# Performance work log

Measured on AMD Instinct MI355X. Metric: run time of the kernel, lower is better.

Reference implementation:

```python
import jax, jax.numpy as jnp
import numpy as np

B, C, H, W = 2, 512, 64, 64
S = 2            # scale_factor
HEADS = 8
GROUPS = 32      # assumed GroupNorm groups for group_norm(in_channels)
DK = C // HEADS
SCALE = 1.0 / DK ** 2   # faithful to source: 1/d_k**2
RES = H // S
R = RES * 2 - 1


def setup_inputs() -> dict:
    key = jax.random.key(0)
    ks = jax.random.split(key, 8)
    f = lambda k, shp, s=0.02: jax.random.normal(k, shp, jnp.float32) * s
    return {
        "x": jax.random.normal(ks[0], (B, C, H, W), jnp.float32),
        "q_w": f(ks[1], (C, C, 1, 1)),
        "q_b": jnp.zeros((C,), jnp.float32),
        "kv_w": f(ks[2], (2 * C, C, 1, 1)),
        "kv_b": jnp.zeros((2 * C,), jnp.float32),
        "off1_w": f(ks[3], (C, C, S, S)),
        "off1_b": jnp.zeros((C,), jnp.float32),
        "gn_w": jnp.ones((C,), jnp.float32),
        "gn_b": jnp.zeros((C,), jnp.float32),
        "off2_w": f(ks[4], (2, C, 1, 1)),
        "rpe_table": f(ks[5], (HEADS, R, R), 0.01),
        "proj_w": f(ks[6], (C, C, 1, 1)),
        "proj_b": jnp.zeros((C,), jnp.float32),
    }


def _conv(x, w, b=None, stride=1):
    y = jax.lax.conv_general_dilated(x, w, (stride, stride), 'VALID',
                                     dimension_numbers=('NCHW', 'OIHW', 'NCHW'))
    return y if b is None else y + b[None, :, None, None]


def _group_norm(x, w, b, eps=1e-5):
    n, c, h, wd = x.shape
    xg = x.reshape(n, GROUPS, -1)
    mu = xg.mean(-1, keepdims=True)
    var = xg.var(-1, keepdims=True)
    xg = (xg - mu) * jax.lax.rsqrt(var + eps)
    return xg.reshape(n, c, h, wd) * w[None, :, None, None] + b[None, :, None, None]


def _grid_sample(img, grid):
    # bilinear, align_corners=True; img [B,C,H,W], grid [B,...,2] in (x,y) order
    Bn, Cn, Hn, Wn = img.shape
    gshape = grid.shape[1:-1]
    g = grid.reshape(Bn, -1, 2)
    x = (g[..., 0] + 1.0) * 0.5 * (Wn - 1)
    y = (g[..., 1] + 1.0) * 0.5 * (Hn - 1)
    x0 = jnp.floor(x); y0 = jnp.floor(y)
    wx = (x - x0)[:, None, :]; wy = (y - y0)[:, None, :]
    x0i = jnp.clip(x0.astype(jnp.int32), 0, Wn - 1)
    x1i = jnp.clip(x0i + 1, 0, Wn - 1)
    y0i = jnp.clip(y0.astype(jnp.int32), 0, Hn - 1)
    y1i = jnp.clip(y0i + 1, 0, Hn - 1)
    imf = img.reshape(Bn, Cn, Hn * Wn)
    gat = lambda yi, xi: jnp.take_along_axis(imf, (yi * Wn + xi)[:, None, :], axis=2)
    out = (gat(y0i, x0i) * (1 - wx) * (1 - wy) + gat(y0i, x1i) * wx * (1 - wy)
           + gat(y1i, x0i) * (1 - wx) * wy + gat(y1i, x1i) * wx * wy)
    return out.reshape(Bn, Cn, *gshape)


def _forward(x, q_w, q_b, kv_w, kv_b, off1_w, off1_b, gn_w, gn_b, off2_w,
             rpe_table, proj_w, proj_b):
    l = H * W
    q = _conv(x, q_w, q_b)                                   # [B,C,H,W]
    t = _conv(q, off1_w, off1_b, stride=S)                   # [B,C,h,w]
    t = jax.nn.gelu(_group_norm(t, gn_w, gn_b), approximate=False)
    offset = _conv(t, off2_w).transpose(0, 2, 3, 1)          # [B,h,w,2] (y,x)
    h, w = offset.shape[1], offset.shape[2]
    n = h * w
    # reference points (linspace 0.5..h-0.5, normalized by h-1)
    ry = (jnp.linspace(0.5, h - 0.5, h) / (h - 1.0)) * 2.0 - 1.0
    rx = (jnp.linspace(0.5, w - 0.5, w) / (w - 1.0)) * 2.0 - 1.0
    ref = jnp.stack(jnp.meshgrid(ry, rx, indexing='ij'), -1)  # [h,w,2]
    pos = jnp.clip(offset + ref[None], -1.0, 1.0)             # [B,h,w,2]
    sampled = _grid_sample(x, pos[..., ::-1])                 # [B,C,h,w] (context=x)
    kv = _conv(sampled.reshape(B, C, 1, n), kv_w, kv_b)       # [B,2C,1,n]
    k, v = kv[:, :C], kv[:, C:]
    qf = q.reshape(B * HEADS, DK, l)
    kf = k.reshape(B * HEADS, DK, n)
    vf = v.reshape(B * HEADS, DK, n)
    attn = jnp.einsum('bcm,bcn->bmn', qf, kf) * SCALE         # [B*H, l, n]
    # query grid (arange, normalized by dim-1)
    gy = jnp.arange(H, dtype=jnp.float32) / (H - 1.0) * 2.0 - 1.0
    gx = jnp.arange(W, dtype=jnp.float32) / (W - 1.0) * 2.0 - 1.0
    qg = jnp.stack(jnp.meshgrid(gy, gx, indexing='ij'), -1).reshape(l, 2)
    disp = (qg[None, :, None, :] - pos.reshape(B, 1, n, 2)) * 0.5  # [B,l,n,2]
    rpe = jnp.broadcast_to(rpe_table[None], (B, HEADS, R, R))
    bias = _grid_sample(rpe, disp[..., ::-1])                  # [B,HEADS,l,n]
    attn = jax.nn.softmax(attn + bias.reshape(B * HEADS, l, n), axis=-1)
    out = jnp.einsum('bmn,bcn->bcm', attn, vf).reshape(B, C, H, W)
    return _conv(out, proj_w, proj_b)


def reference(x, q_w, q_b, kv_w, kv_b, off1_w, off1_b, gn_w, gn_b, off2_w,
              rpe_table, proj_w, proj_b):
    return _forward(x, q_w, q_b, kv_w, kv_b, off1_w, off1_b, gn_w, gn_b,
                    off2_w, rpe_table, proj_w, proj_b)
```

## Files before the change

kernel.cpp:

```cpp
#include <hip/hip_runtime.h>
#include <hip/hip_bf16.h>
#include <hip/hip_fp16.h>
#include <math.h>

typedef float floatx4 __attribute__((ext_vector_type(4)));
typedef short shortx8 __attribute__((ext_vector_type(8)));
typedef unsigned short ush;

#define NB    2
#define NC    512
#define NL    4096
#define NN    1024
#define NH    8
#define NDK   64
#define NR    63
#define LOG2E 1.44269504f
#define QT_SCALE (1.44269504f/4096.0f)

#define OFF_QT     0u
#define OFF_T      2097152u
#define OFF_GS     3145728u
#define OFF_POS    3145856u
#define OFF_KT     3149952u
#define OFF_VV     3674240u
#define OFF_SMP    4198528u
#define OFF_WEFF   4722816u
#define OFF_BEFF   5771392u
#define OFF_PART   5771904u
#define OFF_AO     5771904u

__device__ __forceinline__ ush f2bf(float f) {
    unsigned u = __float_as_uint(f);
    u += 0x7fffu + ((u >> 16) & 1u);
    return (ush)(u >> 16);
}
__device__ __forceinline__ float bf2f(ush h) {
    return __uint_as_float(((unsigned)h) << 16);
}

template<int NP, int BSRC, int OUTMODE>
__global__ __launch_bounds__(256) void gemm_mfma_k(
    const float* __restrict__ A, const void* __restrict__ Bv,
    const float* __restrict__ bias, void* __restrict__ Yv, void* __restrict__ Y2,
    int M, int K, int P, int KS)
{
    __shared__ ush a_hi[128 * 72];
    __shared__ ush b_hi[64 * 72];
    __shared__ ush a_lo[NP == 3 ? 128 * 72 : 64];
    __shared__ ush b_lo[NP == 3 ? 64 * 72 : 64];

    int tid = threadIdx.x;
    int wv = tid >> 6, lane = tid & 63, quad = lane >> 4, l15 = lane & 15;
    int bz = blockIdx.z;
    int b = bz / KS, ks = bz - b * KS;
    int m0 = blockIdx.y * 128, p0 = blockIdx.x * 64;
    int Ksl = K / KS, kbeg = ks * Ksl;

    floatx4 acc[2][4];
    #pragma unroll
    for (int mt = 0; mt < 2; ++mt)
        #pragma unroll
        for (int pt = 0; pt < 4; ++pt) acc[mt][pt] = (floatx4)0.f;

    for (int kc = 0; kc < Ksl; kc += 64) {
        int kg0 = kbeg + kc;
        #pragma unroll
        for (int r = 0; r < 8; ++r) {
            int idx = r * 256 + tid;
            int m = idx >> 4, k4 = (idx & 15) << 2;
            float4 av = *(const float4*)(A + (size_t)(m0 + m) * K + kg0 + k4);
            int o = m * 72 + k4;
            ush h0 = f2bf(av.x), h1 = f2bf(av.y), h2 = f2bf(av.z), h3 = f2bf(av.w);
            a_hi[o] = h0; a_hi[o + 1] = h1; a_hi[o + 2] = h2; a_hi[o + 3] = h3;
            if (NP == 3) {
                a_lo[o]     = f2bf(av.x - bf2f(h0));
                a_lo[o + 1] = f2bf(av.y - bf2f(h1));
                a_lo[o + 2] = f2bf(av.z - bf2f(h2));
                a_lo[o + 3] = f2bf(av.w - bf2f(h3));
            }
        }
        #pragma unroll
        for (int r = 0; r < 8; ++r) {
            int idx = r * 256 + tid;
            int k = idx >> 5, p2 = (idx & 31) << 1;
            float v0, v1;
            if (BSRC == 0) {
                const float* Bp = (const float*)Bv + (size_t)b * K * P;
                float2 t2 = *(const float2*)(Bp + (size_t)(kg0 + k) * P + p0 + p2);
                v0 = t2.x; v1 = t2.y;
            } else if (BSRC == 1) {
                const float* Bp = (const float*)Bv + (size_t)b * NC * NL;
                int kk = kg0 + k;
                int c = kk >> 2, kh = (kk >> 1) & 1, kw = kk & 1;
                int p = p0 + p2;
                int oh = p >> 5, ow = p & 31;
                const float* base = Bp + (size_t)c * NL + (2 * oh + kh) * 64 + kw;
                v0 = base[2 * ow];
                v1 = base[2 * ow + 2];
            } else {
                const ush* Bp = (const ush*)Bv + (size_t)b * K * P;
                unsigned u = *(const unsigned*)(Bp + (size_t)(kg0 + k) * P + p0 + p2);
                v0 = bf2f((ush)(u & 0xffffu));
                v1 = bf2f((ush)(u >> 16));
            }
            ush h0 = f2bf(v0), h1 = f2bf(v1);
            b_hi[p2 * 72 + k] = h0;
            b_hi[(p2 + 1) * 72 + k] = h1;
            if (NP == 3) {
                b_lo[p2 * 72 + k]       = f2bf(v0 - bf2f(h0));
                b_lo[(p2 + 1) * 72 + k] = f2bf(v1 - bf2f(h1));
            }
        }
        __syncthreads();

        shortx8 ah[2][2], al[2][2];
        #pragma unroll
        for (int mt = 0; mt < 2; ++mt)
            #pragma unroll
            for (int kk = 0; kk < 2; ++kk) {
                int o = (wv * 32 + mt * 16 + l15) * 72 + kk * 32 + quad * 8;
                ah[mt][kk] = *(const shortx8*)&a_hi[o];
                if (NP == 3) al[mt][kk] = *(const shortx8*)&a_lo[o];
            }
        #pragma unroll
        for (int pt = 0; pt < 4; ++pt) {
            #pragma unroll
            for (int kk = 0; kk < 2; ++kk) {
                int o = (pt * 16 + l15) * 72 + kk * 32 + quad * 8;
                shortx8 bh = *(const shortx8*)&b_hi[o];
                acc[0][pt] = __builtin_amdgcn_mfma_f32_16x16x32_bf16(ah[0][kk], bh, acc[0][pt], 0, 0, 0);
                acc[1][pt] = __builtin_amdgcn_mfma_f32_16x16x32_bf16(ah[1][kk], bh, acc[1][pt], 0, 0, 0);
                if (NP == 3) {
                    shortx8 bl = *(const shortx8*)&b_lo[o];
                    acc[0][pt] = __builtin_amdgcn_mfma_f32_16x16x32_bf16(ah[0][kk], bl, acc[0][pt], 0, 0, 0);
                    acc[1][pt] = __builtin_amdgcn_mfma_f32_16x16x32_bf16(ah[1][kk], bl, acc[1][pt], 0, 0, 0);
                    acc[0][pt] = __builtin_amdgcn_mfma_f32_16x16x32_bf16(al[0][kk], bh, acc[0][pt], 0, 0, 0);
                    acc[1][pt] = __builtin_amdgcn_mfma_f32_16x16x32_bf16(al[1][kk], bh, acc[1][pt], 0, 0, 0);
                }
            }
        }
        __syncthreads();
    }

    #pragma unroll
    for (int mt = 0; mt < 2; ++mt) {
        #pragma unroll
        for (int reg = 0; reg < 4; ++reg) {
            int m = m0 + wv * 32 + mt * 16 + quad * 4 + reg;
            float bb = (OUTMODE == 2) ? 0.f : bias[m];
            #pragma unroll
            for (int pt = 0; pt < 4; ++pt) {
                int p = p0 + pt * 16 + l15;
                float val = acc[mt][pt][reg] + bb;
                if (OUTMODE == 0) {
                    ((float*)Yv)[(size_t)b * M * P + (size_t)m * P + p] = val;
                } else if (OUTMODE == 2) {
                    ((float*)Yv)[(size_t)(ks * NB + b) * M * P + (size_t)m * P + p] = val;
                } else if (OUTMODE == 5) {
                    int h = m >> 6, d = m & 63;
                    ((ush*)Yv)[(((size_t)(b * 8 + h) * 4096) + p) * 64 + d] = f2bf(val * QT_SCALE);
                } else {
                    if (m < 512) {
                        int h = m >> 6, d = m & 63;
                        ((ush*)Yv)[(((size_t)(b * 8 + h) * 1024) + p) * 64 + d] = f2bf(val);
                    } else {
                        int c = m - 512;
                        ((ush*)Y2)[((size_t)(b * 512) + c) * 1024 + p] = f2bf(val);
                    }
                }
            }
        }
    }
}

__global__ __launch_bounds__(256) void weff_k(
    const float* __restrict__ off1w, const float* __restrict__ qw,
    float* __restrict__ weff)
{
    int ci = blockIdx.x * 256 + threadIdx.x;
    int co0 = blockIdx.y * 4;
    float acc[4][4] = {};
    #pragma unroll 4
    for (int cm = 0; cm < 512; ++cm) {
        float qv = qw[(size_t)cm * 512 + ci];
        #pragma unroll
        for (int c = 0; c < 4; ++c) {
            float4 w4 = *(const float4*)(off1w + ((size_t)(co0 + c) * 512 + cm) * 4);
            acc[c][0] += w4.x * qv;
            acc[c][1] += w4.y * qv;
            acc[c][2] += w4.z * qv;
            acc[c][3] += w4.w * qv;
        }
    }
    #pragma unroll
    for (int c = 0; c < 4; ++c)
        #pragma unroll
        for (int khw = 0; khw < 4; ++khw)
            weff[(size_t)(co0 + c) * 2048 + ci * 4 + khw] = acc[c][khw];
}

__global__ __launch_bounds__(256) void biaseff_k(const float* __restrict__ off1w,
                                                 const float* __restrict__ off1b,
                                                 const float* __restrict__ qb,
                                                 float* __restrict__ beff)
{
    int co = blockIdx.x;
    int tid = threadIdx.x;
    float s = 0.f;
    #pragma unroll
    for (int r = 0; r < 2; ++r) {
        int cm = r * 256 + tid;
        float4 w = *(const float4*)(off1w + ((size_t)co * 512 + cm) * 4);
        s += (w.x + w.y + w.z + w.w) * qb[cm];
    }
    #pragma unroll
    for (int off = 32; off >= 1; off >>= 1) s += __shfl_xor(s, off);
    __shared__ float red[4];
    if ((tid & 63) == 0) red[tid >> 6] = s;
    __syncthreads();
    if (tid == 0) beff[co] = off1b[co] + red[0] + red[1] + red[2] + red[3];
}

__global__ __launch_bounds__(256) void reduce_off1_k(const float* __restrict__ part,
                                                     const float* __restrict__ beff,
                                                     float* __restrict__ t)
{
    int i = blockIdx.x * 256 + threadIdx.x;
    float v = part[i] + part[i + 1048576] + part[i + 2097152] + part[i + 3145728];
    t[i] = v + beff[(i >> 10) & 511];
}

__global__ __launch_bounds__(256) void gn_stats_k(const float* __restrict__ T, float* __restrict__ gs)
{
    int bg = blockIdx.x;
    const float* base = T + (size_t)bg * 16384;
    float s = 0.f, ss = 0.f;
    for (int i = threadIdx.x; i < 16384; i += 256) { float v = base[i]; s += v; ss += v * v; }
    #pragma unroll
    for (int off = 32; off >= 1; off >>= 1) { s += __shfl_xor(s, off); ss += __shfl_xor(ss, off); }
    __shared__ float red[8];
    int wv = threadIdx.x >> 6;
    if ((threadIdx.x & 63) == 0) { red[wv * 2] = s; red[wv * 2 + 1] = ss; }
    __syncthreads();
    if (threadIdx.x == 0) {
        float S = red[0] + red[2] + red[4] + red[6];
        float SS = red[1] + red[3] + red[5] + red[7];
        float mu = S / 16384.f;
        float var = SS / 16384.f - mu * mu;
        gs[bg * 2] = mu;
        gs[bg * 2 + 1] = rsqrtf(var + 1e-5f);
    }
}

__global__ __launch_bounds__(256) void gn_gelu_k(float* __restrict__ T, const float* __restrict__ gs,
                                                 const float* __restrict__ gw, const float* __restrict__ gb)
{
    int idx = blockIdx.x * 256 + threadIdx.x;
    int bg = idx >> 14;
    int c = (idx >> 10) & 511;
    float mu = gs[bg * 2], rs = gs[bg * 2 + 1];
    float v = (T[idx] - mu) * rs * gw[c] + gb[c];
    T[idx] = v * 0.5f * (1.f + erff(v * 0.70710678118654752f));
}

__global__ __launch_bounds__(256) void offset_pos_k(const float* __restrict__ T,
                                                    const float* __restrict__ w2,
                                                    float* __restrict__ pos)
{
    int b = blockIdx.x >> 5;
    int og = threadIdx.x & 31;
    int cg = threadIdx.x >> 5;
    int op = ((blockIdx.x & 31) << 5) + og;
    const float* Tb = T + (size_t)b * NC * NN + (size_t)cg * 64 * NN + op;
    float o0 = 0.f, o1 = 0.f;
    #pragma unroll 4
    for (int c = 0; c < 64; ++c) {
        float tv = Tb[(size_t)c * NN];
        o0 += w2[cg * 64 + c] * tv;
        o1 += w2[512 + cg * 64 + c] * tv;
    }
    __shared__ float rs[2][8][32];
    rs[0][cg][og] = o0;
    rs[1][cg][og] = o1;
    __syncthreads();
    if (threadIdx.x < 64) {
        int coord = threadIdx.x >> 5, og2 = threadIdx.x & 31;
        float s = 0.f;
        #pragma unroll
        for (int k = 0; k < 8; ++k) s += rs[coord][k][og2];
        int opf = ((blockIdx.x & 31) << 5) + og2;
        int oh = opf >> 5, ow = opf & 31;
        float ref = (coord == 0) ? ((0.5f + oh) / 31.f * 2.f - 1.f)
                                 : ((0.5f + ow) / 31.f * 2.f - 1.f);
        pos[((size_t)b * 1024 + opf) * 2 + coord] = fminf(fmaxf(s + ref, -1.f), 1.f);
    }
}

__global__ __launch_bounds__(256) void sample_k(const float* __restrict__ x,
                                                const float* __restrict__ pos,
                                                ush* __restrict__ smp)
{
    int idx = blockIdx.x * 256 + threadIdx.x;
    int j = idx & 1023, c = (idx >> 10) & 511, b = idx >> 19;
    float py = pos[(b * 1024 + j) * 2];
    float px = pos[(b * 1024 + j) * 2 + 1];
    float fx = (px + 1.f) * 0.5f * 63.f;
    float fy = (py + 1.f) * 0.5f * 63.f;
    float flx = floorf(fx), fly = floorf(fy);
    float wx = fx - flx, wy = fy - fly;
    int x0 = min(max((int)flx, 0), 63), y0 = min(max((int)fly, 0), 63);
    int x1 = min(x0 + 1, 63),           y1 = min(y0 + 1, 63);
    const float* xb = x + ((size_t)(b * NC + c)) * NL;
    float v00 = xb[y0 * 64 + x0];
    float v01 = xb[y0 * 64 + x1];
    float v10 = xb[y1 * 64 + x0];
    float v11 = xb[y1 * 64 + x1];
    float v = v00 * (1 - wx) * (1 - wy) + v01 * wx * (1 - wy)
            + v10 * (1 - wx) * wy       + v11 * wx * wy;
    smp[idx] = f2bf(v);
}

__global__ __launch_bounds__(512, 4) void attn_k(
    const ush* __restrict__ qT, const ush* __restrict__ kT,
    const ush* __restrict__ vv, const float* __restrict__ pos,
    const float* __restrict__ rpe, ush* __restrict__ ao)
{
    __shared__ __align__(16) char smem[38912];
    ush*      pa     = (ush*)smem;
    unsigned* tab2_s = (unsigned*)(smem + 18432);
    __half2*  posj_h = (__half2*)(smem + 34816);
    ush*      obuf   = (ush*)smem;

    int bh = blockIdx.y;
    int b = bh >> 3, h = bh & 7;
    int m0 = blockIdx.x * 128;
    int tid = threadIdx.x;
    int wv = tid >> 6, lane = tid & 63, quad = lane >> 4, l15 = lane & 15;

    const ush* qbase = qT + ((size_t)bh * 4096 + m0 + wv * 16 + l15) * 64 + quad * 8;
    shortx8 qf0 = *(const shortx8*)(qbase);
    shortx8 qf1 = *(const shortx8*)(qbase + 32);

    const float* R = rpe + (size_t)h * (NR * NR);
    for (int i = tid; i < 4096; i += 512) {
        int y = i >> 6, xx = i & 63;
        float a = (y < NR && xx < NR)     ? R[y * NR + xx] * LOG2E : 0.f;
        float bv = (y < NR && xx + 1 < NR) ? R[y * NR + xx + 1] * LOG2E : 0.f;
        tab2_s[i] = (unsigned)f2bf(a) | ((unsigned)f2bf(bv) << 16);
    }
    const float2* pb = (const float2*)(pos + (size_t)b * 2048);
    for (int i = tid; i < 1024; i += 512) {
        float2 p = pb[i];
        posj_h[i] = __floats2half2_rn(p.x * 15.5f, p.y * 15.5f);
    }

    float qy15[4], qx15[4];
    #pragma unroll
    for (int reg = 0; reg < 4; ++reg) {
        int mg = m0 + wv * 16 + quad * 4 + reg;
        qy15[reg] = (float)(mg >> 6) * (31.f / 63.f) + 15.5f;
        qx15[reg] = (float)(mg & 63) * (31.f / 63.f) + 15.5f;
    }

    floatx4 o_acc[4], o_sum;
    #pragma unroll
    for (int dt = 0; dt < 4; ++dt) o_acc[dt] = (floatx4)0.f;
    o_sum = (floatx4)0.f;
    shortx8 vone = {16256, 16256, 16256, 16256, 16256, 16256, 16256, 16256};

    __syncthreads();

    const ush* kbase = kT + (size_t)bh * 1024 * 64;
    const ush* vbase = vv + (size_t)(b * 512 + h * 64) * 1024;

    for (int jc = 0; jc < 16; ++jc) {
        int j0 = jc * 64;
        floatx4 sacc[4];
        #pragma unroll
        for (int jt = 0; jt < 4; ++jt) sacc[jt] = (floatx4)0.f;
        #pragma unroll
        for (int jt = 0; jt < 4; ++jt) {
            const ush* kp = kbase + (size_t)(j0 + jt * 16 + l15) * 64 + quad * 8;
            shortx8 kf0 = *(const shortx8*)kp;
            shortx8 kf1 = *(const shortx8*)(kp + 32);
            sacc[jt] = __builtin_amdgcn_mfma_f32_16x16x32_bf16(qf0, kf0, sacc[jt], 0, 0, 0);
            sacc[jt] = __builtin_amdgcn_mfma_f32_16x16x32_bf16(qf1, kf1, sacc[jt], 0, 0, 0);
        }
        shortx8 vf0[4], vf1[4];
        #pragma unroll
        for (int dt = 0; dt < 4; ++dt) {
            const ush* vp = vbase + (size_t)(dt * 16 + l15) * 1024 + j0 + quad * 8;
            vf0[dt] = *(const shortx8*)vp;
            vf1[dt] = *(const shortx8*)(vp + 32);
        }
        #pragma unroll
        for (int jt = 0; jt < 4; ++jt) {
            int j = j0 + jt * 16 + l15;
            float2 pp = __half22float2(posj_h[j]);
            #pragma unroll
            for (int reg = 0; reg < 4; ++reg) {
                float gy = qy15[reg] - pp.x;
                float gx = qx15[reg] - pp.y;
                float fy = floorf(gy), fx = floorf(gx);
                float wy = gy - fy, wx = gx - fx;
                int y0 = min(max((int)fy, 0), 62);
                int x0 = min(max((int)fx, 0), 62);
                unsigned r0 = tab2_s[(y0 << 6) + x0];
                unsigned r1 = tab2_s[((y0 + 1) << 6) + x0];
                float r00 = __uint_as_float(r0 << 16);
                float r01 = __uint_as_float(r0 & 0xffff0000u);
                float r10 = __uint_as_float(r1 << 16);
                float r11 = __uint_as_float(r1 & 0xffff0000u);
                float bx0 = r00 + wx * (r01 - r00);
                float bx1 = r10 + wx * (r11 - r10);
                float p = exp2f(sacc[jt][reg] + (bx0 + wy * (bx1 - bx0)));
                pa[(wv * 16 + quad * 4 + reg) * 72 + jt * 16 + l15] = f2bf(p);
            }
        }
        const ush* pbase = pa + (wv * 16 + l15) * 72 + quad * 8;
        shortx8 pf0 = *(const shortx8*)pbase;
        shortx8 pf1 = *(const shortx8*)(pbase + 32);
        o_sum = __builtin_amdgcn_mfma_f32_16x16x32_bf16(pf0, vone, o_sum, 0, 0, 0);
        o_sum = __builtin_amdgcn_mfma_f32_16x16x32_bf16(pf1, vone, o_sum, 0, 0, 0);
        #pragma unroll
        for (int dt = 0; dt < 4; ++dt) {
            o_acc[dt] = __builtin_amdgcn_mfma_f32_16x16x32_bf16(pf0, vf0[dt], o_acc[dt], 0, 0, 0);
            o_acc[dt] = __builtin_amdgcn_mfma_f32_16x16x32_bf16(pf1, vf1[dt], o_acc[dt], 0, 0, 0);
        }
    }

    __syncthreads();
    float inv[4];
    #pragma unroll
    for (int reg = 0; reg < 4; ++reg) inv[reg] = 1.f / o_sum[reg];
    #pragma unroll
    for (int dt = 0; dt < 4; ++dt)
        #pragma unroll
        for (int reg = 0; reg < 4; ++reg)
            obuf[(dt * 16 + l15) * 136 + wv * 16 + quad * 4 + reg] = f2bf(o_acc[dt][reg] * inv[reg]);
    __syncthreads();
    ush* aobase = ao + ((size_t)(b * 512 + h * 64)) * 4096 + m0;
    for (int i = tid; i < 8192; i += 512) {
        int d = i >> 7, m = i & 127;
        aobase[(size_t)d * 4096 + m] = obuf[d * 136 + m];
    }
}

extern "C" void kernel_launch(void* const* d_in, const int* in_sizes, int n_in,
                              void* d_out, int out_size, void* d_ws, size_t ws_size,
                              hipStream_t stream) {
    const float* x      = (const float*)d_in[0];
    const float* q_w    = (const float*)d_in[1];
    const float* q_b    = (const float*)d_in[2];
    const float* kv_w   = (const float*)d_in[3];
    const float* kv_b   = (const float*)d_in[4];
    const float* off1_w = (const float*)d_in[5];
    const float* off1_b = (const float*)d_in[6];
    const float* gn_w   = (const float*)d_in[7];
    const float* gn_b   = (const float*)d_in[8];
    const float* off2_w = (const float*)d_in[9];
    const float* rpe    = (const float*)d_in[10];
    const float* proj_w = (const float*)d_in[11];
    const float* proj_b = (const float*)d_in[12];

    float* ws   = (float*)d_ws;
    ush*   qT   = (ush*)(ws + OFF_QT);
    float* t    = ws + OFF_T;
    float* gs   = ws + OFF_GS;
    float* pos  = ws + OFF_POS;
    ush*   kT   = (ush*)(ws + OFF_KT);
    ush*   vv   = (ush*)(ws + OFF_VV);
    ush*   smp  = (ush*)(ws + OFF_SMP);
    float* weff = ws + OFF_WEFF;
    float* beff = ws + OFF_BEFF;
    float* part = ws + OFF_PART;
    ush*   ao   = (ush*)(ws + OFF_AO);
    float* out  = (float*)d_out;

    weff_k<<<dim3(2, 128), 256, 0, stream>>>(off1_w, q_w, weff);
    biaseff_k<<<512, 256, 0, stream>>>(off1_w, off1_b, q_b, beff);
    gemm_mfma_k<1, 0, 5><<<dim3(64, 4, 2), 256, 0, stream>>>(q_w, x, q_b, qT, nullptr, 512, 512, 4096, 1);
    gemm_mfma_k<3, 1, 2><<<dim3(16, 4, 8), 256, 0, stream>>>(weff, x, nullptr, part, nullptr, 512, 2048, 1024, 4);
    reduce_off1_k<<<4096, 256, 0, stream>>>(part, beff, t);
    gn_stats_k<<<64, 256, 0, stream>>>(t, gs);
    gn_gelu_k<<<4096, 256, 0, stream>>>(t, gs, gn_w, gn_b);
    offset_pos_k<<<64, 256, 0, stream>>>(t, off2_w, pos);
    sample_k<<<4096, 256, 0, stream>>>(x, pos, smp);
    gemm_mfma_k<1, 2, 4><<<dim3(16, 8, 2), 256, 0, stream>>>(kv_w, smp, kv_b, kT, vv, 1024, 512, 1024, 1);
    attn_k<<<dim3(32, 16), 512, 0, stream>>>(qT, kT, vv, pos, rpe, ao);
    gemm_mfma_k<1, 2, 0><<<dim3(64, 4, 2), 256, 0, stream>>>(proj_w, ao, proj_b, out, nullptr, 512, 512, 4096, 1);
}
```

Measured before the change: 399.6 us.

## Split attention over key halves, combine partials, precompute 4-tap RPE table

The attention kernel now splits the 1024 keys into two halves along a new grid dimension. This doubles the block count to improve occupancy and load balance on the CUs. Each half writes unnormalized bf16 partial outputs and fp32 row denominators, and a new combine kernel sums them and normalizes into the attention output buffer. A separate kernel precomputes a per-head bilinear table with all four RPE taps packed into a uint2, so each bias lookup is one LDS read instead of two; the launch bound also rises to 6 waves. In exchange it adds two launches, extra global traffic for the partials, and bf16 rounding of unnormalized partial sums.

```diff
diff --git a/kernel.cpp b/kernel.cpp
--- a/kernel.cpp
+++ b/kernel.cpp
@@ -18,6 +18,7 @@
 #define QT_SCALE (1.44269504f/4096.0f)
 
 #define OFF_QT     0u
+#define OFF_AO     0u
 #define OFF_T      2097152u
 #define OFF_GS     3145728u
 #define OFF_POS    3145856u
@@ -27,7 +28,9 @@
 #define OFF_WEFF   4722816u
 #define OFF_BEFF   5771392u
 #define OFF_PART   5771904u
-#define OFF_AO     5771904u
+#define OFF_PO0    4198528u
+#define OFF_PDEN   8392832u
+#define OFF_TAB4   8523904u
 
 __device__ __forceinline__ ush f2bf(float f) {
     unsigned u = __float_as_uint(f);
@@ -320,20 +323,39 @@
     smp[idx] = f2bf(v);
 }
 
-__global__ __launch_bounds__(512, 4) void attn_k(
+__global__ __launch_bounds__(256) void tab4_k(const float* __restrict__ rpe,
+                                              uint2* __restrict__ tab4)
+{
+    int i = blockIdx.x * 256 + threadIdx.x;
+    int h = i >> 12, y = (i >> 6) & 63, x = i & 63;
+    const float* R = rpe + (size_t)h * 3969;
+    float v00 = (y < 63 && x < 63)         ? R[y * 63 + x] * LOG2E : 0.f;
+    float v01 = (y < 63 && x + 1 < 63)     ? R[y * 63 + x + 1] * LOG2E : 0.f;
+    float v10 = (y + 1 < 63 && x < 63)     ? R[(y + 1) * 63 + x] * LOG2E : 0.f;
+    float v11 = (y + 1 < 63 && x + 1 < 63) ? R[(y + 1) * 63 + x + 1] * LOG2E : 0.f;
+    uint2 o;
+    o.x = (unsigned)f2bf(v00) | ((unsigned)f2bf(v01) << 16);
+    o.y = (unsigned)f2bf(v10) | ((unsigned)f2bf(v11) << 16);
+    tab4[i] = o;
+}
+
+__global__ __launch_bounds__(512, 6) void attn_k(
     const ush* __restrict__ qT, const ush* __restrict__ kT,
     const ush* __restrict__ vv, const float* __restrict__ pos,
-    const float* __restrict__ rpe, ush* __restrict__ ao)
-{
-    __shared__ __align__(16) char smem[38912];
-    ush*      pa     = (ush*)smem;
-    unsigned* tab2_s = (unsigned*)(smem + 18432);
-    __half2*  posj_h = (__half2*)(smem + 34816);
-    ush*      obuf   = (ush*)smem;
+    const uint2* __restrict__ tab4,
+    ush* __restrict__ po, float* __restrict__ pden)
+{
+    __shared__ __align__(16) char smem[53248];
+    ush*     pa     = (ush*)smem;
+    uint2*   tab_s  = (uint2*)(smem + 18432);
+    __half2* posj_h = (__half2*)(smem + 51200);
+    ush*     obuf   = (ush*)smem;
 
     int bh = blockIdx.y;
     int b = bh >> 3, h = bh & 7;
     int m0 = blockIdx.x * 128;
+    int js = blockIdx.z;
+    int jg = js * 512;
     int tid = threadIdx.x;
     int wv = tid >> 6, lane = tid & 63, quad = lane >> 4, l15 = lane & 15;
 
@@ -341,15 +363,10 @@
     shortx8 qf0 = *(const shortx8*)(qbase);
     shortx8 qf1 = *(const shortx8*)(qbase + 32);
 
-    const float* R = rpe + (size_t)h * (NR * NR);
-    for (int i = tid; i < 4096; i += 512) {
-        int y = i >> 6, xx = i & 63;
-        float a = (y < NR && xx < NR)     ? R[y * NR + xx] * LOG2E : 0.f;
-        float bv = (y < NR && xx + 1 < NR) ? R[y * NR + xx + 1] * LOG2E : 0.f;
-        tab2_s[i] = (unsigned)f2bf(a) | ((unsigned)f2bf(bv) << 16);
-    }
-    const float2* pb = (const float2*)(pos + (size_t)b * 2048);
-    for (int i = tid; i < 1024; i += 512) {
+    const uint2* tg = tab4 + (size_t)h * 4096;
+    for (int i = tid; i < 4096; i += 512) tab_s[i] = tg[i];
+    const float2* pb = (const float2*)(pos + (size_t)b * 2048) + jg;
+    for (int i = tid; i < 512; i += 512) {
         float2 p = pb[i];
         posj_h[i] = __floats2half2_rn(p.x * 15.5f, p.y * 15.5f);
     }
@@ -370,10 +387,10 @@
 
     __syncthreads();
 
-    const ush* kbase = kT + (size_t)bh * 1024 * 64;
-    const ush* vbase = vv + (size_t)(b * 512 + h * 64) * 1024;
-
-    for (int jc = 0; jc < 16; ++jc) {
+    const ush* kbase = kT + ((size_t)bh * 1024 + jg) * 64;
+    const ush* vbase = vv + (size_t)(b * 512 + h * 64) * 1024 + jg;
+
+    for (int jc = 0; jc < 8; ++jc) {
         int j0 = jc * 64;
         floatx4 sacc[4];
         #pragma unroll
@@ -405,12 +422,11 @@
                 float wy = gy - fy, wx = gx - fx;
                 int y0 = min(max((int)fy, 0), 62);
                 int x0 = min(max((int)fx, 0), 62);
-                unsigned r0 = tab2_s[(y0 << 6) + x0];
-                unsigned r1 = tab2_s[((y0 + 1) << 6) + x0];
-                float r00 = __uint_as_float(r0 << 16);
-                float r01 = __uint_as_float(r0 & 0xffff0000u);
-                float r10 = __uint_as_float(r1 << 16);
-                float r11 = __uint_as_float(r1 & 0xffff0000u);
+                uint2 tw = tab_s[(y0 << 6) + x0];
+                float r00 = __uint_as_float(tw.x << 16);
+                float r01 = __uint_as_float(tw.x & 0xffff0000u);
+                float r10 = __uint_as_float(tw.y << 16);
+                float r11 = __uint_as_float(tw.y & 0xffff0000u);
                 float bx0 = r00 + wx * (r01 - r00);
                 float bx1 = r10 + wx * (r11 - r10);
                 float p = exp2f(sacc[jt][reg] + (bx0 + wy * (bx1 - bx0)));
@@ -429,21 +445,37 @@
         }
     }
 
+    if (l15 == 0) {
+        float* pd = pden + ((size_t)(js * 16 + bh) << 12) + m0 + wv * 16 + quad * 4;
+        #pragma unroll
+        for (int reg = 0; reg < 4; ++reg) pd[reg] = o_sum[reg];
+    }
     __syncthreads();
-    float inv[4];
-    #pragma unroll
-    for (int reg = 0; reg < 4; ++reg) inv[reg] = 1.f / o_sum[reg];
     #pragma unroll
     for (int dt = 0; dt < 4; ++dt)
         #pragma unroll
         for (int reg = 0; reg < 4; ++reg)
-            obuf[(dt * 16 + l15) * 136 + wv * 16 + quad * 4 + reg] = f2bf(o_acc[dt][reg] * inv[reg]);
+            obuf[(dt * 16 + l15) * 136 + wv * 16 + quad * 4 + reg] = f2bf(o_acc[dt][reg]);
     __syncthreads();
-    ush* aobase = ao + ((size_t)(b * 512 + h * 64)) * 4096 + m0;
+    ush* pobase = po + (size_t)js * 4194304 + ((size_t)(b * 512 + h * 64)) * 4096 + m0;
     for (int i = tid; i < 8192; i += 512) {
         int d = i >> 7, m = i & 127;
-        aobase[(size_t)d * 4096 + m] = obuf[d * 136 + m];
-    }
+        pobase[(size_t)d * 4096 + m] = obuf[d * 136 + m];
+    }
+}
+
+__global__ __launch_bounds__(256) void combine_k(const ush* __restrict__ po,
+                                                 const float* __restrict__ pden,
+                                                 ush* __restrict__ ao)
+{
+    int idx = blockIdx.x * 256 + threadIdx.x;
+    int m = idx & 4095;
+    int c = (idx >> 12) & 511;
+    int b = idx >> 21;
+    int bh = b * 8 + (c >> 6);
+    float den = pden[((size_t)bh << 12) + m] + pden[((size_t)(16 + bh) << 12) + m];
+    float o = bf2f(po[idx]) + bf2f(po[idx + 4194304]);
+    ao[idx] = f2bf(o / den);
 }
 
 extern "C" void kernel_launch(void* const* d_in, const int* in_sizes, int n_in,
@@ -474,6 +506,9 @@
     float* weff = ws + OFF_WEFF;
     float* beff = ws + OFF_BEFF;
     float* part = ws + OFF_PART;
+    ush*   po   = (ush*)(ws + OFF_PO0);
+    float* pden = ws + OFF_PDEN;
+    uint2* tab4 = (uint2*)(ws + OFF_TAB4);
     ush*   ao   = (ush*)(ws + OFF_AO);
     float* out  = (float*)d_out;
 
@@ -485,8 +520,10 @@
     gn_stats_k<<<64, 256, 0, stream>>>(t, gs);
     gn_gelu_k<<<4096, 256, 0, stream>>>(t, gs, gn_w, gn_b);
     offset_pos_k<<<64, 256, 0, stream>>>(t, off2_w, pos);
+    tab4_k<<<128, 256, 0, stream>>>(rpe, tab4);
     sample_k<<<4096, 256, 0, stream>>>(x, pos, smp);
     gemm_mfma_k<1, 2, 4><<<dim3(16, 8, 2), 256, 0, stream>>>(kv_w, smp, kv_b, kT, vv, 1024, 512, 1024, 1);
-    attn_k<<<dim3(32, 16), 512, 0, stream>>>(qT, kT, vv, pos, rpe, ao);
+    attn_k<<<dim3(32, 16, 2), 512, 0, stream>>>(qT, kT, vv, pos, tab4, po, pden);
+    combine_k<<<16384, 256, 0, stream>>>(po, pden, ao);
     gemm_mfma_k<1, 2, 0><<<dim3(64, 4, 2), 256, 0, stream>>>(proj_w, ao, proj_b, out, nullptr, 512, 512, 4096, 1);
 }
```

Result: slower. 422.7 us (+5.8%).
